# Kernel optimization log

Hardware: AMD Instinct MI355X
Metric: run time of the kernel (lower is better)

The kernel has to match this reference:

```python
import jax, jax.numpy as jnp
import numpy as np
from jax import lax

CURRICULUM_EP = 12
LI, LS, LW = 0.5, 0.8, 3.0


def _gauss_win(ws, C, dtype):
    coords = jnp.arange(ws, dtype=jnp.float32) - ws // 2
    g = jnp.exp(-coords ** 2 / (2 * 1.5 ** 2))
    win = g[None, :] * g[:, None]
    win = win / win.sum()
    # depthwise kernel, OIHW with I=1, O=C
    return jnp.broadcast_to(win[None, None], (C, 1, ws, ws)).astype(dtype)


def _dwconv(x, win, p, C):
    return lax.conv_general_dilated(
        x, win, window_strides=(1, 1), padding=[(p, p), (p, p)],
        dimension_numbers=('NCHW', 'OIHW', 'NCHW'), feature_group_count=C)


def diff_ssim(x, y, ws=11):
    C1, C2 = 0.01 ** 2, 0.03 ** 2
    C = x.shape[1]
    p = ws // 2
    win = _gauss_win(ws, C, x.dtype)
    mx = _dwconv(x, win, p, C)
    my = _dwconv(y, win, p, C)
    sxx = _dwconv(x * x, win, p, C) - mx ** 2
    syy = _dwconv(y * y, win, p, C) - my ** 2
    sxy = _dwconv(x * y, win, p, C) - mx * my
    ssim_map = (2 * mx * my + C1) * (2 * sxy + C2) / ((mx ** 2 + my ** 2 + C1) * (sxx + syy + C2))
    return ssim_map.mean()


def setup_inputs() -> dict:
    key = jax.random.key(0)
    k1, k2, k3, k4 = jax.random.split(key, 4)
    B, C, H, W = 16, 3, 512, 512
    NB = 1024  # watermark bits
    eps = 1e-4
    cover = jax.random.uniform(k1, (B, C, H, W), dtype=jnp.float32)
    wmed = jax.random.uniform(k2, (B, C, H, W), dtype=jnp.float32)
    wm_orig = jax.random.uniform(k3, (B, NB), dtype=jnp.float32)
    wm_ext = jnp.clip(jax.random.uniform(k4, (B, NB), dtype=jnp.float32), eps, 1.0 - eps)
    return {"cover": cover, "wmed": wmed, "wm_orig": wm_orig, "wm_ext": wm_ext, "epoch": 20}


def reference(cover, wmed, wm_orig, wm_ext, epoch):
    ml = jnp.mean((wmed - cover) ** 2)
    sv = diff_ssim(wmed, cover)
    sl = 1.0 - sv
    wl = jnp.mean(-(wm_orig * jnp.log(wm_ext) + (1.0 - wm_orig) * jnp.log(1.0 - wm_ext)))
    if epoch <= CURRICULUM_EP:
        w_img, w_ssim = 0.05, 0.05
    else:
        progress = min(1.0, (epoch - CURRICULUM_EP) / 10.0)
        w_img = 0.05 + (LI - 0.05) * progress
        w_ssim = 0.05 + (LS - 0.05) * progress
    total = w_img * ml + w_ssim * sl + LW * wl
    return (total, ml, sv, wl)
```

## Files before the change

kernel.cpp:

```cpp
#include <hip/hip_runtime.h>
#include <math.h>

#define H_IMG 512
#define W_IMG 512
#define HALO 5
#define WS11 11
#define NTHREADS 256
#define NCHUNK 16

#define SLOTS 64
#define RS 36
#define FS (SLOTS*RS)
#define RBUF_N (5*FS)

typedef float f2 __attribute__((ext_vector_type(2)));

__host__ __device__ constexpr float WT(int t) {
    return (t==0||t==10) ? 0.00102838f :
           (t==1||t==9)  ? 0.00759873f :
           (t==2||t==8)  ? 0.03600075f :
           (t==3||t==7)  ? 0.10936070f :
           (t==4||t==6)  ? 0.21300556f :
           (t==5)        ? 0.26601172f : 0.0f;
}

static __device__ __forceinline__ f2 splat2(float v) { f2 r = {v, v}; return r; }

static __device__ __forceinline__ void hconv_row(
        const float* __restrict__ xp, const float* __restrict__ yp,
        float* __restrict__ rbuf, int g, int c0, int bx, bool xin,
        float& mse_acc) {
    const bool rok = (unsigned)g < (unsigned)H_IMG;
    const int gc = bx*32 + c0 - 5;
    float xv[14], yv[14];
    if (rok && xin) {
        const int ga = gc - 3;
        const float* rx = xp + (size_t)g*W_IMG + ga;
        const float* ry = yp + (size_t)g*W_IMG + ga;
        float4 XA = *(const float4*)(rx);
        float4 XB = *(const float4*)(rx + 4);
        float4 XC = *(const float4*)(rx + 8);
        float4 XD = *(const float4*)(rx + 12);
        float  XE = rx[16];
        float4 YA = *(const float4*)(ry);
        float4 YB = *(const float4*)(ry + 4);
        float4 YC = *(const float4*)(ry + 8);
        float4 YD = *(const float4*)(ry + 12);
        float  YE = ry[16];
        xv[0]=XA.w;  xv[1]=XB.x;  xv[2]=XB.y;  xv[3]=XB.z;  xv[4]=XB.w;
        xv[5]=XC.x;  xv[6]=XC.y;  xv[7]=XC.z;  xv[8]=XC.w;  xv[9]=XD.x;
        xv[10]=XD.y; xv[11]=XD.z; xv[12]=XD.w; xv[13]=XE;
        yv[0]=YA.w;  yv[1]=YB.x;  yv[2]=YB.y;  yv[3]=YB.z;  yv[4]=YB.w;
        yv[5]=YC.x;  yv[6]=YC.y;  yv[7]=YC.z;  yv[8]=YC.w;  yv[9]=YD.x;
        yv[10]=YD.y; yv[11]=YD.z; yv[12]=YD.w; yv[13]=YE;
    } else if (rok) {
        const float* prx = xp + (size_t)g*W_IMG + gc;
        const float* pry = yp + (size_t)g*W_IMG + gc;
#pragma unroll
        for (int j = 0; j < 14; ++j) {
            bool ok = (unsigned)(gc + j) < (unsigned)W_IMG;
            xv[j] = ok ? prx[j] : 0.f;
            yv[j] = ok ? pry[j] : 0.f;
        }
    } else {
#pragma unroll
        for (int j = 0; j < 14; ++j) { xv[j] = 0.f; yv[j] = 0.f; }
    }

    if (rok) {
#pragma unroll
        for (int j = 5; j < 9; ++j) {
            float d = xv[j] - yv[j];
            mse_acc = fmaf(d, d, mse_acc);
        }
    }

    f2 A[5][2];
#pragma unroll
    for (int f = 0; f < 5; ++f) { A[f][0] = splat2(0.f); A[f][1] = splat2(0.f); }
#pragma unroll
    for (int j = 0; j < 14; ++j) {
        float px = xv[j], py = yv[j];
        f2 vp = {px, py};
        f2 vsq = vp * vp;
        float pxy = px * py;
#pragma unroll
        for (int p = 0; p < 2; ++p) {
            const int t0 = j - 2*p;
            if (t0 >= 0 && t0 <= WS11) {
                const f2 wp = {WT(t0), WT(t0-1)};
                A[0][p] = __builtin_elementwise_fma(wp, splat2(px),    A[0][p]);
                A[1][p] = __builtin_elementwise_fma(wp, splat2(py),    A[1][p]);
                A[2][p] = __builtin_elementwise_fma(wp, splat2(vsq.x), A[2][p]);
                A[3][p] = __builtin_elementwise_fma(wp, splat2(vsq.y), A[3][p]);
                A[4][p] = __builtin_elementwise_fma(wp, splat2(pxy),   A[4][p]);
            }
        }
    }
    const int slot = (g + 5) & (SLOTS-1);
    float* wb = &rbuf[slot*RS + c0];
#pragma unroll
    for (int f = 0; f < 5; ++f) {
        *(float4*)(wb + f*FS) =
            make_float4(A[f][0].x, A[f][0].y, A[f][1].x, A[f][1].y);
    }
}

__global__ __launch_bounds__(NTHREADS, 3) void ssim_stream(
        const float* __restrict__ cover, const float* __restrict__ wmed,
        float* __restrict__ part, int nParts) {
    __shared__ __align__(16) float rbuf[RBUF_N];
    __shared__ float red[8];

    const int tid = threadIdx.x;
    const int bx = blockIdx.x & 15;
    const int pl = blockIdx.x >> 4;
    const size_t pbase = (size_t)pl * (H_IMG*W_IMG);
    const float* xp = wmed + pbase;
    const float* yp = cover + pbase;
    const bool xin = (bx != 0) && (bx != 15);

    float ssim_acc = 0.f, mse_acc = 0.f;

    if (tid < 80) {
        hconv_row(xp, yp, rbuf, (tid >> 3) - 5, (tid & 7) << 2, bx, xin, mse_acc);
    }
    __syncthreads();

    int kbase = 0;
#pragma clang loop unroll(disable)
    for (int k = 0; k < NCHUNK; ++k, kbase += 32) {
        {
            const int r_local = tid >> 3;
            const int c0 = (tid & 7) << 2;
            hconv_row(xp, yp, rbuf, kbase + 5 + r_local, c0, bx, xin, mse_acc);
        }
        __syncthreads();

        if (((tid >> 7) & 1) == (k & 1)) {
            const int s  = tid & 127;
            const int c  = s & 31;
            const int r0 = (s >> 5) << 3;
            int idx[18];
#pragma unroll
            for (int i = 0; i < 18; ++i) {
                int sl = (kbase + r0 + i) & (SLOTS-1);
                idx[i] = sl*RS + c;
            }
            f2 acc2[5][4];
#pragma unroll
            for (int f = 0; f < 5; ++f)
#pragma unroll
                for (int p = 0; p < 4; ++p) acc2[f][p] = splat2(0.f);
#pragma unroll
            for (int f = 0; f < 5; ++f) {
#pragma unroll
                for (int i = 0; i < 18; ++i) {
                    float v = rbuf[f*FS + idx[i]];
#pragma unroll
                    for (int p = 0; p < 4; ++p) {
                        const int t0 = i - 2*p;
                        if (t0 >= 0 && t0 <= WS11) {
                            const f2 wp = {WT(t0), WT(t0-1)};
                            acc2[f][p] = __builtin_elementwise_fma(wp, splat2(v), acc2[f][p]);
                        }
                    }
                }
            }
            const f2 c1 = {0.01f*0.01f, 0.01f*0.01f};
            const f2 c2 = {0.03f*0.03f, 0.03f*0.03f};
            const f2 two = {2.f, 2.f};
#pragma unroll
            for (int p = 0; p < 4; ++p) {
                f2 mx = acc2[0][p], my = acc2[1][p];
                f2 sxx = acc2[2][p] - mx*mx;
                f2 syy = acc2[3][p] - my*my;
                f2 sxy = acc2[4][p] - mx*my;
                f2 num = (two*mx*my + c1) * (two*sxy + c2);
                f2 den = (mx*mx + my*my + c1) * (sxx + syy + c2);
                ssim_acc += __fdividef(num.x, den.x) + __fdividef(num.y, den.y);
            }
        }
        __syncthreads();
    }

#pragma unroll
    for (int off = 32; off > 0; off >>= 1) {
        ssim_acc += __shfl_down(ssim_acc, off);
        mse_acc  += __shfl_down(mse_acc, off);
    }
    int wid = tid >> 6, lane = tid & 63;
    if (lane == 0) { red[wid] = ssim_acc; red[4+wid] = mse_acc; }
    __syncthreads();
    if (tid == 0) {
        float sv = red[0]+red[1]+red[2]+red[3];
        float m  = red[4]+red[5]+red[6]+red[7];
        part[blockIdx.x] = sv;
        part[nParts + blockIdx.x] = m;
    }
}

#define FT 1024
__global__ __launch_bounds__(FT) void finalize_k(
        const float* __restrict__ part, int nParts,
        const float* __restrict__ wm_orig, const float* __restrict__ wm_ext,
        int nWm, const int* __restrict__ epoch_p,
        float* __restrict__ out, double inv_npix, double inv_nwm) {
    __shared__ double red[48];
    int tid = threadIdx.x;
    double s_ssim = 0.0, s_mse = 0.0, s_wl = 0.0;
    const float4* s4 = (const float4*)part;
    const float4* m4 = (const float4*)(part + nParts);
    int n4 = nParts >> 2;
    for (int i = tid; i < n4; i += FT) {
        float4 v = s4[i];
        s_ssim += (double)((v.x + v.y) + (v.z + v.w));
        float4 u = m4[i];
        s_mse  += (double)((u.x + u.y) + (u.z + u.w));
    }
    const float4* p4 = (const float4*)wm_orig;
    const float4* q4 = (const float4*)wm_ext;
    int w4 = nWm >> 2;
    for (int i = tid; i < w4; i += FT) {
        float4 p = p4[i], q = q4[i];
        float a;
        a  = -(p.x*__logf(q.x) + (1.f-p.x)*__logf(1.f-q.x));
        a += -(p.y*__logf(q.y) + (1.f-p.y)*__logf(1.f-q.y));
        a += -(p.z*__logf(q.z) + (1.f-p.z)*__logf(1.f-q.z));
        a += -(p.w*__logf(q.w) + (1.f-p.w)*__logf(1.f-q.w));
        s_wl += (double)a;
    }
#pragma unroll
    for (int off = 32; off > 0; off >>= 1) {
        s_ssim += __shfl_down(s_ssim, off);
        s_mse  += __shfl_down(s_mse, off);
        s_wl   += __shfl_down(s_wl, off);
    }
    int wid = tid >> 6, lane = tid & 63;
    if (lane == 0) { red[wid] = s_ssim; red[16+wid] = s_mse; red[32+wid] = s_wl; }
    __syncthreads();
    if (tid == 0) {
        double ssim_sum = 0.0, mse_sum = 0.0, wl_sum = 0.0;
        for (int i = 0; i < 16; ++i) {
            ssim_sum += red[i]; mse_sum += red[16+i]; wl_sum += red[32+i];
        }
        float sv = (float)(ssim_sum * inv_npix);
        float ml = (float)(mse_sum  * inv_npix);
        float wl = (float)(wl_sum   * inv_nwm);
        int e = *epoch_p;
        float w_img, w_ssim;
        if (e <= 12) {
            w_img = 0.05f; w_ssim = 0.05f;
        } else {
            float progress = fminf(1.0f, (float)(e - 12) / 10.0f);
            w_img  = 0.05f + (0.5f - 0.05f)*progress;
            w_ssim = 0.05f + (0.8f - 0.05f)*progress;
        }
        float sl = 1.0f - sv;
        float total = w_img*ml + w_ssim*sl + 3.0f*wl;
        out[0] = total;
        out[1] = ml;
        out[2] = sv;
        out[3] = wl;
    }
}

extern "C" void kernel_launch(void* const* d_in, const int* in_sizes, int n_in,
                              void* d_out, int out_size, void* d_ws, size_t ws_size,
                              hipStream_t stream) {
    const float* cover   = (const float*)d_in[0];
    const float* wmed    = (const float*)d_in[1];
    const float* wm_orig = (const float*)d_in[2];
    const float* wm_ext  = (const float*)d_in[3];
    const int*   epoch   = (const int*)d_in[4];
    float* out = (float*)d_out;

    int npix   = in_sizes[0];
    int planes = npix / (H_IMG * W_IMG);
    int nWm    = in_sizes[2];

    int nBlocks = 16 * planes;
    int nParts  = nBlocks;
    float* part = (float*)d_ws;

    ssim_stream<<<nBlocks, NTHREADS, 0, stream>>>(cover, wmed, part, nParts);
    finalize_k<<<1, FT, 0, stream>>>(part, nParts, wm_orig, wm_ext, nWm,
                                     epoch, out,
                                     1.0 / (double)npix, 1.0 / (double)nWm);
}
```

Measured before the change: 193.9 us.

## Split each image column strip into four vertical tiles for more blocks

Each block now covers a 32-wide by 128-tall tile instead of a full 512-row column strip, so the grid grows fourfold (3072 blocks). The vertical pass now runs on all 256 threads every iteration instead of alternating halves, and the ring buffer shrinks to 48 slots so occupancy can rise to 4 blocks per CU. The goal is better GPU fill and less idle time. The cost is recomputing 10 halo rows of the horizontal pass per tile, plus an extra prologue per block.

```diff
diff --git a/kernel.cpp b/kernel.cpp
--- a/kernel.cpp
+++ b/kernel.cpp
@@ -3,12 +3,14 @@
 
 #define H_IMG 512
 #define W_IMG 512
+#define TH 32
+#define TW 32
 #define HALO 5
 #define WS11 11
 #define NTHREADS 256
-#define NCHUNK 16
-
-#define SLOTS 64
+#define TPB 4
+
+#define SLOTS 48
 #define RS 36
 #define FS (SLOTS*RS)
 #define RBUF_N (5*FS)
@@ -26,12 +28,12 @@
 
 static __device__ __forceinline__ f2 splat2(float v) { f2 r = {v, v}; return r; }
 
-static __device__ __forceinline__ void hconv_row(
+static __device__ __forceinline__ void hconv_task(
         const float* __restrict__ xp, const float* __restrict__ yp,
-        float* __restrict__ rbuf, int g, int c0, int bx, bool xin,
-        float& mse_acc) {
+        float* __restrict__ rbuf, int g, int slot, int c0, int tx0,
+        bool xin, bool owned, float& mse_acc) {
     const bool rok = (unsigned)g < (unsigned)H_IMG;
-    const int gc = bx*32 + c0 - 5;
+    const int gc = tx0 + c0;
     float xv[14], yv[14];
     if (rok && xin) {
         const int ga = gc - 3;
@@ -67,7 +69,7 @@
         for (int j = 0; j < 14; ++j) { xv[j] = 0.f; yv[j] = 0.f; }
     }
 
-    if (rok) {
+    if (rok && owned) {
 #pragma unroll
         for (int j = 5; j < 9; ++j) {
             float d = xv[j] - yv[j];
@@ -97,7 +99,6 @@
             }
         }
     }
-    const int slot = (g + 5) & (SLOTS-1);
     float* wb = &rbuf[slot*RS + c0];
 #pragma unroll
     for (int f = 0; f < 5; ++f) {
@@ -106,7 +107,7 @@
     }
 }
 
-__global__ __launch_bounds__(NTHREADS, 3) void ssim_stream(
+__global__ __launch_bounds__(NTHREADS, 4) void ssim_mse_tile(
         const float* __restrict__ cover, const float* __restrict__ wmed,
         float* __restrict__ part, int nParts) {
     __shared__ __align__(16) float rbuf[RBUF_N];
@@ -114,51 +115,67 @@
 
     const int tid = threadIdx.x;
     const int bx = blockIdx.x & 15;
-    const int pl = blockIdx.x >> 4;
+    const int yq = (blockIdx.x >> 4) & 3;
+    const int pl = blockIdx.x >> 6;
     const size_t pbase = (size_t)pl * (H_IMG*W_IMG);
     const float* xp = wmed + pbase;
     const float* yp = cover + pbase;
+    const int by0 = yq * (TPB*TH);
+    const int tx0 = bx*TW - HALO;
     const bool xin = (bx != 0) && (bx != 15);
 
     float ssim_acc = 0.f, mse_acc = 0.f;
 
-    if (tid < 80) {
-        hconv_row(xp, yp, rbuf, (tid >> 3) - 5, (tid & 7) << 2, bx, xin, mse_acc);
-    }
-    __syncthreads();
-
-    int kbase = 0;
+    const int rr = tid >> 3;
+    const int c0 = (tid & 7) << 2;
+
 #pragma clang loop unroll(disable)
-    for (int k = 0; k < NCHUNK; ++k, kbase += 32) {
+    for (int it = 0; it < TPB; ++it) {
+        int base = it << 5;
+        if (base >= 48) base -= 48;
+
+        if (it == 0) {
+            {
+                const int r_loc = rr;
+                const int rho = r_loc - 5;
+                hconv_task(xp, yp, rbuf, by0 + rho, r_loc, c0, tx0, xin,
+                           rho >= 0, mse_acc);
+            }
+            if (tid < 80) {
+                const int r_loc = 32 + rr;
+                const int rho = r_loc - 5;
+                hconv_task(xp, yp, rbuf, by0 + rho, r_loc, c0, tx0, xin,
+                           true, mse_acc);
+            }
+        } else {
+            const int rho = (it << 5) + 5 + rr;
+            int slot = base + 10 + rr;
+            if (slot >= 48) slot -= 48;
+            hconv_task(xp, yp, rbuf, by0 + rho, slot, c0, tx0, xin,
+                       rho <= 127, mse_acc);
+        }
+        __syncthreads();
+
         {
-            const int r_local = tid >> 3;
-            const int c0 = (tid & 7) << 2;
-            hconv_row(xp, yp, rbuf, kbase + 5 + r_local, c0, bx, xin, mse_acc);
-        }
-        __syncthreads();
-
-        if (((tid >> 7) & 1) == (k & 1)) {
-            const int s  = tid & 127;
-            const int c  = s & 31;
-            const int r0 = (s >> 5) << 3;
-            int idx[18];
-#pragma unroll
-            for (int i = 0; i < 18; ++i) {
-                int sl = (kbase + r0 + i) & (SLOTS-1);
+            const int c  = tid & 31;
+            const int r0 = (tid >> 5) << 2;
+            int idx[14];
+#pragma unroll
+            for (int i = 0; i < 14; ++i) {
+                int sl = base + r0 + i;
+                if (sl >= 48) sl -= 48;
                 idx[i] = sl*RS + c;
             }
-            f2 acc2[5][4];
-#pragma unroll
-            for (int f = 0; f < 5; ++f)
-#pragma unroll
-                for (int p = 0; p < 4; ++p) acc2[f][p] = splat2(0.f);
+            f2 acc2[5][2];
+#pragma unroll
+            for (int f = 0; f < 5; ++f) { acc2[f][0] = splat2(0.f); acc2[f][1] = splat2(0.f); }
 #pragma unroll
             for (int f = 0; f < 5; ++f) {
 #pragma unroll
-                for (int i = 0; i < 18; ++i) {
+                for (int i = 0; i < 14; ++i) {
                     float v = rbuf[f*FS + idx[i]];
 #pragma unroll
-                    for (int p = 0; p < 4; ++p) {
+                    for (int p = 0; p < 2; ++p) {
                         const int t0 = i - 2*p;
                         if (t0 >= 0 && t0 <= WS11) {
                             const f2 wp = {WT(t0), WT(t0-1)};
@@ -171,7 +188,7 @@
             const f2 c2 = {0.03f*0.03f, 0.03f*0.03f};
             const f2 two = {2.f, 2.f};
 #pragma unroll
-            for (int p = 0; p < 4; ++p) {
+            for (int p = 0; p < 2; ++p) {
                 f2 mx = acc2[0][p], my = acc2[1][p];
                 f2 sxx = acc2[2][p] - mx*mx;
                 f2 syy = acc2[3][p] - my*my;
@@ -193,9 +210,9 @@
     if (lane == 0) { red[wid] = ssim_acc; red[4+wid] = mse_acc; }
     __syncthreads();
     if (tid == 0) {
-        float sv = red[0]+red[1]+red[2]+red[3];
-        float m  = red[4]+red[5]+red[6]+red[7];
-        part[blockIdx.x] = sv;
+        float s = red[0]+red[1]+red[2]+red[3];
+        float m = red[4]+red[5]+red[6]+red[7];
+        part[blockIdx.x] = s;
         part[nParts + blockIdx.x] = m;
     }
 }
@@ -279,11 +296,11 @@
     int planes = npix / (H_IMG * W_IMG);
     int nWm    = in_sizes[2];
 
-    int nBlocks = 16 * planes;
+    int nBlocks = 16 * 4 * planes;
     int nParts  = nBlocks;
     float* part = (float*)d_ws;
 
-    ssim_stream<<<nBlocks, NTHREADS, 0, stream>>>(cover, wmed, part, nParts);
+    ssim_mse_tile<<<nBlocks, NTHREADS, 0, stream>>>(cover, wmed, part, nParts);
     finalize_k<<<1, FT, 0, stream>>>(part, nParts, wm_orig, wm_ext, nWm,
                                      epoch, out,
                                      1.0 / (double)npix, 1.0 / (double)nWm);
```

After: 184.1 us. -5.0%, faster.
